# Performance work log

Measured on AMD Instinct MI355X. Metric: run time of the kernel, lower is better.

Reference implementation:

```python
import jax, jax.numpy as jnp
import numpy as np
import math

B, NMAX, PE, E, DS, NF = 8, 128, 64, 5, 64, 8  # E = num_edge_features + 1


def setup_inputs() -> dict:
    key = jax.random.key(0)
    ks = jax.random.split(key, 10)
    total = B * NMAX
    x = jax.random.normal(ks[0], (total, PE), jnp.float32)
    batch = jnp.arange(total, dtype=jnp.int32) // NMAX  # sorted graph ids, full graphs
    q = jax.random.uniform(ks[1], (B,), jnp.float32, 0.1, 0.9)  # keep sin(2*pi*q) away from 0
    s = 0.05
    return dict(
        x=x, batch=batch, q=q,
        w_attn=jax.random.normal(ks[2], (PE, 4 * E * PE), jnp.float32) * s,
        b_attn=jnp.zeros((4 * E * PE,), jnp.float32),
        w_node=jax.random.normal(ks[3], (PE, NF), jnp.float32) * s,
        b_node=jnp.zeros((NF,), jnp.float32),
        w_phi=jax.random.normal(ks[4], (DS,), jnp.float32) * s,   # Linear(1, DS) weight
        b_phi=jax.random.normal(ks[5], (DS,), jnp.float32) * s,
        w_ctx=jax.random.normal(ks[6], (DS, DS), jnp.float32) * s,  # Linear(DS, DS, bias=False)
        w_self=jax.random.normal(ks[7], (DS,), jnp.float32) * s,  # Linear(1, DS) weight
        b_self=jax.random.normal(ks[8], (DS,), jnp.float32) * s,
        w_out=jax.random.normal(ks[9], (DS,), jnp.float32) * s,   # Linear(DS, 1) weight
        b_out=jnp.zeros((), jnp.float32),
    )


def _to_dense(batch, vals, n_graphs, n_max):
    # torch_geometric.to_dense_batch for sorted batch vector
    starts = jnp.searchsorted(batch, jnp.arange(n_graphs, dtype=batch.dtype))
    pos = jnp.arange(batch.shape[0]) - starts[batch]
    dense = jnp.zeros((n_graphs, n_max, vals.shape[-1]), vals.dtype).at[batch, pos].set(vals)
    mask = jnp.zeros((n_graphs, n_max), bool).at[batch, pos].set(True)
    return dense, mask


def reference(x, batch, q, w_attn, b_attn, w_node, b_node,
              w_phi, b_phi, w_ctx, w_self, b_self, w_out, b_out):
    scale = 1.0 / math.sqrt(E * PE)
    x_hat = x @ w_node + b_node                              # (total, NF)
    proj = x @ w_attn + b_attn                               # (total, 4*E*PE)
    dense, mask = _to_dense(batch, proj, B, NMAX)            # (B, N, 4*E*PE), (B, N)
    k1, q1, k2, q2 = jnp.split(dense, 4, axis=-1)
    heads = lambda t: t.reshape(B, NMAX, E, PE).transpose(0, 2, 1, 3)  # (B, E, N, PE)
    k1, q1, k2, q2 = heads(k1), heads(q1), heads(k2), heads(q2)
    z_re = jnp.einsum('bend,bemd->benm', k1, q1) * scale     # (B, E, N, N)
    z_im = jnp.einsum('bend,bemd->benm', k2, q2) * scale
    c = jnp.cos(2.0 * math.pi * q)[:, None, None, None]
    s = jnp.sin(2.0 * math.pi * q)[:, None, None, None]
    z = z_re + z_im * (2.0 - c) / s                          # (B, E, N, N)
    eye = jnp.eye(NMAX, dtype=bool)
    edge_mask = mask[:, :, None] & mask[:, None, :] & ~eye   # (B, N, N)
    # DeepSetClassifier
    zt = z[..., None]                                        # (B, E, N, N, 1)
    phi_out = zt * w_phi + b_phi                             # (B, E, N, N, DS)
    m = edge_mask[:, None, :, :, None].astype(z.dtype)       # (B, 1, N, N, 1)
    denom = jnp.maximum(edge_mask.sum(-1).astype(z.dtype), 1.0)[:, None, :, None]  # (B,1,N,1)
    ctx = (m * phi_out).sum(3) / denom                       # (B, E, N, DS) masked neighbor mean
    h = jax.nn.gelu(zt * w_self + b_self + (ctx @ w_ctx)[:, :, :, None, :],
                    approximate=False)                        # (B, E, N, N, DS)
    e = (h * w_out).sum(-1) + b_out                          # (B, E, N, N)
    e_hat = jnp.transpose(e, (0, 3, 2, 1))                   # transpose(-1, 1) -> (B, N, N, E)
    return (e_hat, x_hat, edge_mask, mask)
```

## Files before the change

### kernel.cpp

```cpp
#include <hip/hip_runtime.h>
#include <hip/hip_bf16.h>

#define NB 8
#define NMAXN 128
#define PEH 64
#define NE 5
#define DSZ 64
#define NFEAT 8
#define TOTALN 1024
#define PCOLS 1280

#define OUT_XHAT (NB*NMAXN*NMAXN*NE)
#define OUT_EM   (OUT_XHAT + TOTALN*NFEAT)
#define OUT_MASK (OUT_EM + NB*NMAXN*NMAXN)


__global__ void k_fused1(const float* __restrict__ x, const float* __restrict__ qv,
                         const float* __restrict__ w_attn, const float* __restrict__ b_attn,
                         const float* __restrict__ w_node, const float* __restrict__ b_node,
                         const float* __restrict__ w_phi, const float* __restrict__ b_phi,
                         const float* __restrict__ w_ctx, const float* __restrict__ b_self,
                         float* __restrict__ ws, float* __restrict__ out,
                         int offZbar, int offWpc, int offC1, int offFac, int doProj)
{
    int blk = blockIdx.x, t = threadIdx.x;
    if (blk < 256) {
        if (!doProj) return;
        __shared__ float xs[4 * 64];
        int r0 = blk * 4;
        if (t < 256) xs[t] = x[r0 * PEH + t];
        __syncthreads();
        float4 b4 = *(const float4*)&b_attn[4 * t];
        float4 a0 = b4, a1 = b4, a2 = b4, a3 = b4;
        const float* wp = w_attn + 4 * t;
        #pragma unroll 4
        for (int k = 0; k < 64; k++) {
            float4 w4 = *(const float4*)&wp[k * PCOLS];
            float x0 = xs[k], x1 = xs[64 + k], x2 = xs[128 + k], x3 = xs[192 + k];
            a0.x = fmaf(x0, w4.x, a0.x); a0.y = fmaf(x0, w4.y, a0.y); a0.z = fmaf(x0, w4.z, a0.z); a0.w = fmaf(x0, w4.w, a0.w);
            a1.x = fmaf(x1, w4.x, a1.x); a1.y = fmaf(x1, w4.y, a1.y); a1.z = fmaf(x1, w4.z, a1.z); a1.w = fmaf(x1, w4.w, a1.w);
            a2.x = fmaf(x2, w4.x, a2.x); a2.y = fmaf(x2, w4.y, a2.y); a2.z = fmaf(x2, w4.z, a2.z); a2.w = fmaf(x2, w4.w, a2.w);
            a3.x = fmaf(x3, w4.x, a3.x); a3.y = fmaf(x3, w4.y, a3.y); a3.z = fmaf(x3, w4.z, a3.z); a3.w = fmaf(x3, w4.w, a3.w);
        }
        float* pr = ws + r0 * PCOLS + 4 * t;
        *(float4*)&pr[0]         = a0;
        *(float4*)&pr[PCOLS]     = a1;
        *(float4*)&pr[2 * PCOLS] = a2;
        *(float4*)&pr[3 * PCOLS] = a3;
        return;
    }
    int b2 = blk - 256;
    if (b2 < 32) {
        if (t < 256) {
            int g = b2 * 256 + t;
            int row = g >> 3, f = g & 7;
            const float* xr = x + row * PEH;
            float acc = b_node[f];
            #pragma unroll 8
            for (int k = 0; k < PEH; k++) acc = fmaf(xr[k], w_node[k * NFEAT + f], acc);
            out[OUT_XHAT + g] = acc;
        }
    } else if (b2 < 48) {
        int base = (b2 - 32) * 8192;
        for (int g = base + t; g < base + 8192; g += 320) {
            int n = (g >> 7) & 127, m = g & 127;
            out[OUT_EM + g] = (n == m) ? 0.0f : 1.0f;
        }
    } else if (b2 == 48) {
        for (int g = t; g < 1024; g += 320) out[OUT_MASK + g] = 1.0f;
    } else if (b2 == 49) {
        if (t < 64) {
            float wpv = 0.f, bpv = 0.f;
            for (int i = 0; i < 64; i++) {
                float wc = w_ctx[i * 64 + t];
                wpv = fmaf(w_phi[i], wc, wpv);
                bpv = fmaf(b_phi[i], wc, bpv);
            }
            ws[offWpc + t] = wpv;
            ws[offC1 + t]  = b_self[t] + bpv;
        } else if (t < 72) {
            int b = t - 64;
            float qq = qv[b];
            float ang = 6.2831853071795864f * qq;
            float c = cosf(ang), s = sinf(ang);
            ws[offFac + b] = (2.0f - c) / s;
        }
    } else {
        int base = (b2 - 50) * 2560;
        for (int g = t; g < 2560; g += 320) ws[offZbar + base + g] = 0.0f;
    }
}

__global__ void k_z_fast(float* __restrict__ ws, int zsF, int offZbar, int offFac)
{
    __shared__ alignas(16) float sm[8192 + 1280 + 1024];
    float* smA = sm;
    float* smQ = sm + 8192;
    float* zp  = sm + 8192 + 1280;

    int t = threadIdx.x;
    int blk = blockIdx.x;
    int ms = blk & 7, be = blk >> 3;
    int b = be / 5, e = be - 5 * b;
    float fac = ws[offFac + b];
    const float scale = 0.05590169943749474f;
    float sfac = scale * fac;

    const float* proj = ws;
    int kn = t >> 1, kkb = (t & 1) * 32;
    int qm = t & 15, qkb = (t >> 4) * 4;

    int tx = t & 7, ty = t >> 3;
    int m0 = 2 * tx, n0 = 4 * ty;
    float acc[4][2] = {};

    for (int pass = 0; pass < 2; pass++) {
        __syncthreads();
        int colK = (pass ? 640 : 0)   + e * 64;
        int colQ = (pass ? 960 : 320) + e * 64;
        float sc = pass ? sfac : scale;
        const float* prK = proj + (b * NMAXN + kn) * PCOLS + colK + kkb;
        #pragma unroll
        for (int j4 = 0; j4 < 8; j4++) {
            float4 v = *(const float4*)&prK[4 * j4];
            smA[(kkb + 4*j4 + 0) * 128 + kn] = sc * v.x;
            smA[(kkb + 4*j4 + 1) * 128 + kn] = sc * v.y;
            smA[(kkb + 4*j4 + 2) * 128 + kn] = sc * v.z;
            smA[(kkb + 4*j4 + 3) * 128 + kn] = sc * v.w;
        }
        const float* prQ = proj + (b * NMAXN + ms * 16 + qm) * PCOLS + colQ + qkb;
        {
            float4 v = *(const float4*)&prQ[0];
            smQ[(qkb + 0) * 20 + qm] = v.x;
            smQ[(qkb + 1) * 20 + qm] = v.y;
            smQ[(qkb + 2) * 20 + qm] = v.z;
            smQ[(qkb + 3) * 20 + qm] = v.w;
        }
        __syncthreads();
        for (int k = 0; k < 64; k++) {
            float4 a4 = *(const float4*)&smA[k * 128 + n0];
            float2 q2 = *(const float2*)&smQ[k * 20 + m0];
            float ar[4] = {a4.x, a4.y, a4.z, a4.w};
            #pragma unroll
            for (int r = 0; r < 4; r++) {
                acc[r][0] = fmaf(ar[r], q2.x, acc[r][0]);
                acc[r][1] = fmaf(ar[r], q2.y, acc[r][1]);
            }
        }
    }
    __syncthreads();

    __hip_bfloat16* zsb = (__hip_bfloat16*)(ws + zsF);
    float psum[4] = {0.f, 0.f, 0.f, 0.f};
    #pragma unroll
    for (int c = 0; c < 2; c++) {
        int mg = ms * 16 + m0 + c;
        union { ushort4 u; __hip_bfloat16 h[4]; } pk;
        #pragma unroll
        for (int r = 0; r < 4; r++) {
            pk.h[r] = __float2bfloat16(acc[r][c]);
            if (mg != n0 + r) psum[r] += acc[r][c];
        }
        *(ushort4*)&zsb[((b * NMAXN + mg) * NE + e) * NMAXN + n0] = pk.u;
    }
    #pragma unroll
    for (int r = 0; r < 4; r++) zp[(n0 + r) * 8 + tx] = psum[r];
    __syncthreads();
    if (t < 128) {
        float s = 0.f;
        #pragma unroll
        for (int xx = 0; xx < 8; xx++) s += zp[t * 8 + xx];
        atomicAdd(&ws[offZbar + (b * NE + e) * NMAXN + t], s);
    }
}

__device__ __forceinline__ float gelu_fast(float x) {
    float x2 = x * x;
    float w  = -1.5957691216057308f * x * fmaf(0.044715f, x2, 1.0f);
    float ew = __expf(w);
    return x * __builtin_amdgcn_rcpf(1.0f + ew);
}

__global__ void k_epi(const float* __restrict__ ws, const float* __restrict__ w_self,
                      const float* __restrict__ w_out, const float* __restrict__ b_out,
                      float* __restrict__ out,
                      int zsF, int offZbar, int offWpc, int offC1)
{
    __shared__ alignas(16) float4 cwi[64];
    int t = threadIdx.x;
    int b = blockIdx.x >> 6, mp = blockIdx.x & 63;
    int m0 = 2 * mp;
    if (t < 64)
        cwi[t] = make_float4(w_self[t], ws[offWpc + t], ws[offC1 + t], w_out[t]);
    float zbv = ws[offZbar + b * 640 + t] * (1.0f / 127.0f);
    __syncthreads();

    const __hip_bfloat16* zsb = (const __hip_bfloat16*)(ws + zsF);
    int e = t >> 7, n = t & 127;
    float zv0 = __bfloat162float(zsb[(b * NMAXN + m0) * 640 + t]);
    float zv1 = __bfloat162float(zsb[(b * NMAXN + m0 + 1) * 640 + t]);
    float bo = b_out[0];
    float a0 = bo, a1 = bo;
    #pragma unroll 8
    for (int d = 0; d < 64; d++) {
        float4 c = cwi[d];
        float zc = fmaf(zbv, c.y, c.z);
        a0 = fmaf(gelu_fast(fmaf(zv0, c.x, zc)), c.w, a0);
        a1 = fmaf(gelu_fast(fmaf(zv1, c.x, zc)), c.w, a1);
    }
    int oo = n * NE + e;
    out[(b * NMAXN + m0) * 640 + oo]     = a0;
    out[(b * NMAXN + m0 + 1) * 640 + oo] = a1;
}

__device__ __forceinline__ void z_store4(float acc[4][4], float* ws, float* zp,
                                         int zsF, int offZbar,
                                         int b, int e, int mq, int t)
{
    int tx = t & 7, ty = t >> 3;
    int m0 = 4 * tx, n0 = 4 * ty;
    __hip_bfloat16* zsb = (__hip_bfloat16*)(ws + zsF);
    float psum[4] = {0.f, 0.f, 0.f, 0.f};
    #pragma unroll
    for (int c = 0; c < 4; c++) {
        int mg = mq * 32 + m0 + c;
        union { ushort4 u; __hip_bfloat16 h[4]; } pk;
        #pragma unroll
        for (int r = 0; r < 4; r++) {
            pk.h[r] = __float2bfloat16(acc[r][c]);
            if (mg != n0 + r) psum[r] += acc[r][c];
        }
        *(ushort4*)&zsb[((b * NMAXN + mg) * NE + e) * NMAXN + n0] = pk.u;
    }
    #pragma unroll
    for (int r = 0; r < 4; r++) zp[(n0 + r) * 8 + tx] = psum[r];
    __syncthreads();
    if (t < 128) {
        float s = 0.f;
        #pragma unroll
        for (int xx = 0; xx < 8; xx++) s += zp[t * 8 + xx];
        atomicAdd(&ws[offZbar + (b * NE + e) * NMAXN + t], s);
    }
}

__global__ void k_z_slow(const float* __restrict__ x, const float* __restrict__ w_attn,
                         const float* __restrict__ b_attn, float* __restrict__ ws,
                         int zsF, int offZbar, int offFac)
{
    __shared__ alignas(16) float sm[8320 + 2304 + 1024];
    float* xsm = sm;
    float* smA = sm;
    float* smQ = sm + 8320;
    float* zp  = sm + 8320 + 2304;

    int t = threadIdx.x;
    int blk = blockIdx.x;
    int mq = blk & 3, be = blk >> 2;
    int b = be / 5, e = be - 5 * b;
    float fac = ws[offFac + b];
    const float scale = 0.05590169943749474f;
    float sfac = scale * fac;

    int kn   = t >> 1;
    int kkb  = (t & 1) * 32;
    int qm   = t & 31;
    int qkb  = (t >> 5) * 8;
    int mglo = mq * 32 + qm;

    int tx = t & 7, ty = t >> 3;
    int m0 = 4 * tx, n0 = 4 * ty;
    float acc[4][4] = {};

    for (int pass = 0; pass < 2; pass++) {
        __syncthreads();
        for (int i = t; i < 128 * 16; i += 256) {
            int n = i >> 4, dd = (i & 15) * 4;
            float4 xv = *(const float4*)&x[(b * NMAXN + n) * PEH + dd];
            float* dst = &xsm[n * 65 + dd];
            dst[0] = xv.x; dst[1] = xv.y; dst[2] = xv.z; dst[3] = xv.w;
        }
        __syncthreads();
        int colK = (pass ? 640 : 0)   + e * 64 + kkb;
        int colQ = (pass ? 960 : 320) + e * 64 + qkb;
        float rk[32], rq[8];
        #pragma unroll
        for (int j = 0; j < 32; j++) rk[j] = b_attn[colK + j];
        #pragma unroll
        for (int j = 0; j < 8; j++)  rq[j] = b_attn[colQ + j];
        for (int d = 0; d < 64; d++) {
            const float* wrow = w_attn + d * PCOLS;
            float xk = xsm[kn * 65 + d];
            float xq = xsm[mglo * 65 + d];
            #pragma unroll
            for (int j4 = 0; j4 < 8; j4++) {
                float4 w4 = *(const float4*)&wrow[colK + 4 * j4];
                rk[4*j4+0] = fmaf(xk, w4.x, rk[4*j4+0]);
                rk[4*j4+1] = fmaf(xk, w4.y, rk[4*j4+1]);
                rk[4*j4+2] = fmaf(xk, w4.z, rk[4*j4+2]);
                rk[4*j4+3] = fmaf(xk, w4.w, rk[4*j4+3]);
            }
            #pragma unroll
            for (int j4 = 0; j4 < 2; j4++) {
                float4 w4 = *(const float4*)&wrow[colQ + 4 * j4];
                rq[4*j4+0] = fmaf(xq, w4.x, rq[4*j4+0]);
                rq[4*j4+1] = fmaf(xq, w4.y, rq[4*j4+1]);
                rq[4*j4+2] = fmaf(xq, w4.z, rq[4*j4+2]);
                rq[4*j4+3] = fmaf(xq, w4.w, rq[4*j4+3]);
            }
        }
        __syncthreads();
        float sc = pass ? sfac : scale;
        #pragma unroll
        for (int j = 0; j < 32; j++) smA[(kkb + j) * 128 + kn] = sc * rk[j];
        #pragma unroll
        for (int j = 0; j < 8; j++)  smQ[(qkb + j) * 36 + qm] = rq[j];
        __syncthreads();
        for (int k = 0; k < 64; k++) {
            float4 a4 = *(const float4*)&smA[k * 128 + n0];
            float4 q4 = *(const float4*)&smQ[k * 36 + m0];
            float ar[4] = {a4.x, a4.y, a4.z, a4.w};
            float qr[4] = {q4.x, q4.y, q4.z, q4.w};
            #pragma unroll
            for (int r = 0; r < 4; r++)
                #pragma unroll
                for (int c = 0; c < 4; c++)
                    acc[r][c] = fmaf(ar[r], qr[c], acc[r][c]);
        }
    }
    __syncthreads();
    z_store4(acc, ws, zp, zsF, offZbar, b, e, mq, t);
}

__global__ void k_epi_slow(const float* __restrict__ ws, const float* __restrict__ w_self,
                           const float* __restrict__ w_out, const float* __restrict__ b_out,
                           float* __restrict__ out,
                           int zsF, int offZbar, int offWpc, int offC1)
{
    __shared__ alignas(16) float4 cwi[64];
    int t = threadIdx.x;
    int b = blockIdx.x >> 7, m = blockIdx.x & 127;
    if (t < 64)
        cwi[t] = make_float4(w_self[t], ws[offWpc + t], ws[offC1 + t], w_out[t]);
    float zbv = ws[offZbar + b * 640 + t] * (1.0f / 127.0f);
    __syncthreads();

    const __hip_bfloat16* zsb = (const __hip_bfloat16*)(ws + zsF);
    int e = t >> 7, n = t & 127;
    float zv = __bfloat162float(zsb[(b * NMAXN + m) * 640 + t]);
    float acc = b_out[0];
    #pragma unroll 8
    for (int d = 0; d < 64; d++) {
        float4 c = cwi[d];
        float arg = fmaf(zv, c.x, fmaf(zbv, c.y, c.z));
        acc = fmaf(gelu_fast(arg), c.w, acc);
    }
    out[(b * NMAXN + m) * 640 + n * NE + e] = acc;
}

extern "C" void kernel_launch(void* const* d_in, const int* in_sizes, int n_in,
                              void* d_out, int out_size, void* d_ws, size_t ws_size,
                              hipStream_t stream)
{
    const float* x      = (const float*)d_in[0];
    const float* q      = (const float*)d_in[2];
    const float* w_attn = (const float*)d_in[3];
    const float* b_attn = (const float*)d_in[4];
    const float* w_node = (const float*)d_in[5];
    const float* b_node = (const float*)d_in[6];
    const float* w_phi  = (const float*)d_in[7];
    const float* b_phi  = (const float*)d_in[8];
    const float* w_ctx  = (const float*)d_in[9];
    const float* w_self = (const float*)d_in[10];
    const float* b_self = (const float*)d_in[11];
    const float* w_out  = (const float*)d_in[12];
    const float* b_out  = (const float*)d_in[13];
    float* ws  = (float*)d_ws;
    float* out = (float*)d_out;

    const bool big = ws_size >= (size_t)(1643656 * 4 + 64);
    const int zsF     = big ? (TOTALN * PCOLS) : 0;
    const int offZbar = zsF + 327680;
    const int offWpc  = offZbar + 5120;
    const int offC1   = offWpc + 64;
    const int offFac  = offC1 + 64;

    k_fused1<<<308, 320, 0, stream>>>(x, q, w_attn, b_attn, w_node, b_node,
                                      w_phi, b_phi, w_ctx, b_self,
                                      ws, out, offZbar, offWpc, offC1, offFac, big ? 1 : 0);
    if (big) {
        k_z_fast<<<320, 256, 0, stream>>>(ws, zsF, offZbar, offFac);
        k_epi<<<512, 640, 0, stream>>>(ws, w_self, w_out, b_out, out,
                                       zsF, offZbar, offWpc, offC1);
    } else {
        k_z_slow<<<160, 256, 0, stream>>>(x, w_attn, b_attn, ws, zsF, offZbar, offFac);
        k_epi_slow<<<1024, 640, 0, stream>>>(ws, w_self, w_out, b_out, out,
                                             zsF, offZbar, offWpc, offC1);
    }
}
```

Measured before the change: 119.0 us.

## Fuse projection into z kernel and drop separate projection/setup launch

Removes the standalone projection GEMM pass and the separate z kernel. A single 193-block kernel now recomputes the K/Q projection per (batch, edge, quarter) tile from x and w_attn in registers, and also produces x_hat and the masks. Per-quarter neighbour sums are written to separate slots instead of atomically added, which removes the zero-init pass. The ctx weight precompute moves into the epilogue kernel. This cuts the launch count from three to two and avoids the round trip of the projection buffer through global memory, at the cost of redundant projection arithmetic across the m-quarters.

New measurement: 193.1 us. +62.2%, slower.

```diff
diff --git a/kernel.cpp b/kernel.cpp
--- a/kernel.cpp
+++ b/kernel.cpp
@@ -14,132 +14,104 @@
 #define OUT_EM   (OUT_XHAT + TOTALN*NFEAT)
 #define OUT_MASK (OUT_EM + NB*NMAXN*NMAXN)
 
-
-__global__ void k_fused1(const float* __restrict__ x, const float* __restrict__ qv,
-                         const float* __restrict__ w_attn, const float* __restrict__ b_attn,
-                         const float* __restrict__ w_node, const float* __restrict__ b_node,
-                         const float* __restrict__ w_phi, const float* __restrict__ b_phi,
-                         const float* __restrict__ w_ctx, const float* __restrict__ b_self,
-                         float* __restrict__ ws, float* __restrict__ out,
-                         int offZbar, int offWpc, int offC1, int offFac, int doProj)
+#define OFF_ZBAR 327680
+#define ZBAR_STRIDE 5120
+
+__global__ __launch_bounds__(512)
+void k_zfused(const float* __restrict__ x, const float* __restrict__ qv,
+              const float* __restrict__ w_attn, const float* __restrict__ b_attn,
+              const float* __restrict__ w_node, const float* __restrict__ b_node,
+              float* __restrict__ ws, float* __restrict__ out)
 {
     int blk = blockIdx.x, t = threadIdx.x;
-    if (blk < 256) {
-        if (!doProj) return;
-        __shared__ float xs[4 * 64];
-        int r0 = blk * 4;
-        if (t < 256) xs[t] = x[r0 * PEH + t];
-        __syncthreads();
-        float4 b4 = *(const float4*)&b_attn[4 * t];
-        float4 a0 = b4, a1 = b4, a2 = b4, a3 = b4;
-        const float* wp = w_attn + 4 * t;
-        #pragma unroll 4
-        for (int k = 0; k < 64; k++) {
-            float4 w4 = *(const float4*)&wp[k * PCOLS];
-            float x0 = xs[k], x1 = xs[64 + k], x2 = xs[128 + k], x3 = xs[192 + k];
-            a0.x = fmaf(x0, w4.x, a0.x); a0.y = fmaf(x0, w4.y, a0.y); a0.z = fmaf(x0, w4.z, a0.z); a0.w = fmaf(x0, w4.w, a0.w);
-            a1.x = fmaf(x1, w4.x, a1.x); a1.y = fmaf(x1, w4.y, a1.y); a1.z = fmaf(x1, w4.z, a1.z); a1.w = fmaf(x1, w4.w, a1.w);
-            a2.x = fmaf(x2, w4.x, a2.x); a2.y = fmaf(x2, w4.y, a2.y); a2.z = fmaf(x2, w4.z, a2.z); a2.w = fmaf(x2, w4.w, a2.w);
-            a3.x = fmaf(x3, w4.x, a3.x); a3.y = fmaf(x3, w4.y, a3.y); a3.z = fmaf(x3, w4.z, a3.z); a3.w = fmaf(x3, w4.w, a3.w);
-        }
-        float* pr = ws + r0 * PCOLS + 4 * t;
-        *(float4*)&pr[0]         = a0;
-        *(float4*)&pr[PCOLS]     = a1;
-        *(float4*)&pr[2 * PCOLS] = a2;
-        *(float4*)&pr[3 * PCOLS] = a3;
-        return;
-    }
-    int b2 = blk - 256;
-    if (b2 < 32) {
-        if (t < 256) {
-            int g = b2 * 256 + t;
+    if (blk >= 160) {
+        int b2 = blk - 160;
+        if (b2 < 16) {
+            int g = b2 * 512 + t;
             int row = g >> 3, f = g & 7;
             const float* xr = x + row * PEH;
             float acc = b_node[f];
             #pragma unroll 8
             for (int k = 0; k < PEH; k++) acc = fmaf(xr[k], w_node[k * NFEAT + f], acc);
             out[OUT_XHAT + g] = acc;
-        }
-    } else if (b2 < 48) {
-        int base = (b2 - 32) * 8192;
-        for (int g = base + t; g < base + 8192; g += 320) {
-            int n = (g >> 7) & 127, m = g & 127;
-            out[OUT_EM + g] = (n == m) ? 0.0f : 1.0f;
-        }
-    } else if (b2 == 48) {
-        for (int g = t; g < 1024; g += 320) out[OUT_MASK + g] = 1.0f;
-    } else if (b2 == 49) {
-        if (t < 64) {
-            float wpv = 0.f, bpv = 0.f;
-            for (int i = 0; i < 64; i++) {
-                float wc = w_ctx[i * 64 + t];
-                wpv = fmaf(w_phi[i], wc, wpv);
-                bpv = fmaf(b_phi[i], wc, bpv);
+        } else if (b2 < 32) {
+            int base = (b2 - 16) * 8192;
+            for (int g = base + t; g < base + 8192; g += 512) {
+                int n = (g >> 7) & 127, m = g & 127;
+                out[OUT_EM + g] = (n == m) ? 0.0f : 1.0f;
             }
-            ws[offWpc + t] = wpv;
-            ws[offC1 + t]  = b_self[t] + bpv;
-        } else if (t < 72) {
-            int b = t - 64;
-            float qq = qv[b];
-            float ang = 6.2831853071795864f * qq;
-            float c = cosf(ang), s = sinf(ang);
-            ws[offFac + b] = (2.0f - c) / s;
-        }
-    } else {
-        int base = (b2 - 50) * 2560;
-        for (int g = t; g < 2560; g += 320) ws[offZbar + base + g] = 0.0f;
-    }
-}
-
-__global__ void k_z_fast(float* __restrict__ ws, int zsF, int offZbar, int offFac)
-{
-    __shared__ alignas(16) float sm[8192 + 1280 + 1024];
+        } else {
+            for (int g = t; g < 1024; g += 512) out[OUT_MASK + g] = 1.0f;
+        }
+        return;
+    }
+
+    __shared__ alignas(16) float sm[8320 + 2304];
+    float* xsm = sm;
     float* smA = sm;
-    float* smQ = sm + 8192;
-    float* zp  = sm + 8192 + 1280;
-
-    int t = threadIdx.x;
-    int blk = blockIdx.x;
-    int ms = blk & 7, be = blk >> 3;
+    float* smQ = sm + 8320;
+    float* zp  = sm + 8320;
+
+    int be = blk >> 2, mq = blk & 3;
     int b = be / 5, e = be - 5 * b;
-    float fac = ws[offFac + b];
+    float ang = 6.2831853071795864f * qv[b];
+    float fac = (2.0f - cosf(ang)) / sinf(ang);
     const float scale = 0.05590169943749474f;
     float sfac = scale * fac;
 
-    const float* proj = ws;
-    int kn = t >> 1, kkb = (t & 1) * 32;
-    int qm = t & 15, qkb = (t >> 4) * 4;
-
-    int tx = t & 7, ty = t >> 3;
+    int kn = t >> 2, kkb = (t & 3) * 16;
+    int qm = t & 31, qkb = (t >> 5) * 4;
+    int qrow = mq * 32 + qm;
+
+    int tx = t & 15, ty = t >> 4;
     int m0 = 2 * tx, n0 = 4 * ty;
     float acc[4][2] = {};
 
     for (int pass = 0; pass < 2; pass++) {
         __syncthreads();
-        int colK = (pass ? 640 : 0)   + e * 64;
-        int colQ = (pass ? 960 : 320) + e * 64;
+        for (int i = t; i < 128 * 16; i += 512) {
+            int n = i >> 4, dd = (i & 15) * 4;
+            float4 xv = *(const float4*)&x[(b * NMAXN + n) * PEH + dd];
+            float* dst = &xsm[n * 65 + dd];
+            dst[0] = xv.x; dst[1] = xv.y; dst[2] = xv.z; dst[3] = xv.w;
+        }
+        __syncthreads();
+        int cK = (pass ? 640 : 0)   + e * 64 + kkb;
+        int cQ = (pass ? 960 : 320) + e * 64 + qkb;
+        float rk[16], rq[4];
+        #pragma unroll
+        for (int j = 0; j < 16; j++) rk[j] = b_attn[cK + j];
+        #pragma unroll
+        for (int j = 0; j < 4; j++)  rq[j] = b_attn[cQ + j];
+        #pragma unroll 4
+        for (int d = 0; d < 64; d++) {
+            const float* wr = w_attn + d * PCOLS;
+            float xk = xsm[kn * 65 + d];
+            float xq = xsm[qrow * 65 + d];
+            #pragma unroll
+            for (int j4 = 0; j4 < 4; j4++) {
+                float4 w4 = *(const float4*)&wr[cK + 4 * j4];
+                rk[4*j4+0] = fmaf(xk, w4.x, rk[4*j4+0]);
+                rk[4*j4+1] = fmaf(xk, w4.y, rk[4*j4+1]);
+                rk[4*j4+2] = fmaf(xk, w4.z, rk[4*j4+2]);
+                rk[4*j4+3] = fmaf(xk, w4.w, rk[4*j4+3]);
+            }
+            float4 wq = *(const float4*)&wr[cQ];
+            rq[0] = fmaf(xq, wq.x, rq[0]);
+            rq[1] = fmaf(xq, wq.y, rq[1]);
+            rq[2] = fmaf(xq, wq.z, rq[2]);
+            rq[3] = fmaf(xq, wq.w, rq[3]);
+        }
+        __syncthreads();
         float sc = pass ? sfac : scale;
-        const float* prK = proj + (b * NMAXN + kn) * PCOLS + colK + kkb;
-        #pragma unroll
-        for (int j4 = 0; j4 < 8; j4++) {
-            float4 v = *(const float4*)&prK[4 * j4];
-            smA[(kkb + 4*j4 + 0) * 128 + kn] = sc * v.x;
-            smA[(kkb + 4*j4 + 1) * 128 + kn] = sc * v.y;
-            smA[(kkb + 4*j4 + 2) * 128 + kn] = sc * v.z;
-            smA[(kkb + 4*j4 + 3) * 128 + kn] = sc * v.w;
-        }
-        const float* prQ = proj + (b * NMAXN + ms * 16 + qm) * PCOLS + colQ + qkb;
-        {
-            float4 v = *(const float4*)&prQ[0];
-            smQ[(qkb + 0) * 20 + qm] = v.x;
-            smQ[(qkb + 1) * 20 + qm] = v.y;
-            smQ[(qkb + 2) * 20 + qm] = v.z;
-            smQ[(qkb + 3) * 20 + qm] = v.w;
-        }
+        #pragma unroll
+        for (int j = 0; j < 16; j++) smA[(kkb + j) * 128 + kn] = sc * rk[j];
+        #pragma unroll
+        for (int j = 0; j < 4; j++)  smQ[(qkb + j) * 36 + qm] = rq[j];
         __syncthreads();
         for (int k = 0; k < 64; k++) {
             float4 a4 = *(const float4*)&smA[k * 128 + n0];
-            float2 q2 = *(const float2*)&smQ[k * 20 + m0];
+            float2 q2 = *(const float2*)&smQ[k * 36 + m0];
             float ar[4] = {a4.x, a4.y, a4.z, a4.w};
             #pragma unroll
             for (int r = 0; r < 4; r++) {
@@ -150,11 +122,11 @@
     }
     __syncthreads();
 
-    __hip_bfloat16* zsb = (__hip_bfloat16*)(ws + zsF);
+    __hip_bfloat16* zsb = (__hip_bfloat16*)ws;
     float psum[4] = {0.f, 0.f, 0.f, 0.f};
     #pragma unroll
     for (int c = 0; c < 2; c++) {
-        int mg = ms * 16 + m0 + c;
+        int mg = mq * 32 + m0 + c;
         union { ushort4 u; __hip_bfloat16 h[4]; } pk;
         #pragma unroll
         for (int r = 0; r < 4; r++) {
@@ -164,13 +136,13 @@
         *(ushort4*)&zsb[((b * NMAXN + mg) * NE + e) * NMAXN + n0] = pk.u;
     }
     #pragma unroll
-    for (int r = 0; r < 4; r++) zp[(n0 + r) * 8 + tx] = psum[r];
+    for (int r = 0; r < 4; r++) zp[(n0 + r) * 16 + tx] = psum[r];
     __syncthreads();
     if (t < 128) {
         float s = 0.f;
         #pragma unroll
-        for (int xx = 0; xx < 8; xx++) s += zp[t * 8 + xx];
-        atomicAdd(&ws[offZbar + (b * NE + e) * NMAXN + t], s);
+        for (int xx = 0; xx < 16; xx++) s += zp[t * 16 + xx];
+        ws[OFF_ZBAR + mq * ZBAR_STRIDE + (b * NE + e) * NMAXN + t] = s;
     }
 }
 
@@ -181,21 +153,33 @@
     return x * __builtin_amdgcn_rcpf(1.0f + ew);
 }
 
-__global__ void k_epi(const float* __restrict__ ws, const float* __restrict__ w_self,
+__global__ void k_epi(const float* __restrict__ ws,
+                      const float* __restrict__ w_phi, const float* __restrict__ b_phi,
+                      const float* __restrict__ w_ctx,
+                      const float* __restrict__ w_self, const float* __restrict__ b_self,
                       const float* __restrict__ w_out, const float* __restrict__ b_out,
-                      float* __restrict__ out,
-                      int zsF, int offZbar, int offWpc, int offC1)
+                      float* __restrict__ out)
 {
     __shared__ alignas(16) float4 cwi[64];
     int t = threadIdx.x;
     int b = blockIdx.x >> 6, mp = blockIdx.x & 63;
     int m0 = 2 * mp;
-    if (t < 64)
-        cwi[t] = make_float4(w_self[t], ws[offWpc + t], ws[offC1 + t], w_out[t]);
-    float zbv = ws[offZbar + b * 640 + t] * (1.0f / 127.0f);
+    if (t < 64) {
+        float wpv = 0.f, bpv = 0.f;
+        #pragma unroll 8
+        for (int i = 0; i < 64; i++) {
+            float wc = w_ctx[i * 64 + t];
+            wpv = fmaf(w_phi[i], wc, wpv);
+            bpv = fmaf(b_phi[i], wc, bpv);
+        }
+        cwi[t] = make_float4(w_self[t], wpv, b_self[t] + bpv, w_out[t]);
+    }
+    const float* zb = ws + OFF_ZBAR + b * 640 + t;
+    float zbv = (zb[0] + zb[ZBAR_STRIDE] + zb[2 * ZBAR_STRIDE] + zb[3 * ZBAR_STRIDE])
+                * (1.0f / 127.0f);
     __syncthreads();
 
-    const __hip_bfloat16* zsb = (const __hip_bfloat16*)(ws + zsF);
+    const __hip_bfloat16* zsb = (const __hip_bfloat16*)ws;
     int e = t >> 7, n = t & 127;
     float zv0 = __bfloat162float(zsb[(b * NMAXN + m0) * 640 + t]);
     float zv1 = __bfloat162float(zsb[(b * NMAXN + m0 + 1) * 640 + t]);
@@ -211,150 +195,6 @@
     int oo = n * NE + e;
     out[(b * NMAXN + m0) * 640 + oo]     = a0;
     out[(b * NMAXN + m0 + 1) * 640 + oo] = a1;
-}
-
-__device__ __forceinline__ void z_store4(float acc[4][4], float* ws, float* zp,
-                                         int zsF, int offZbar,
-                                         int b, int e, int mq, int t)
-{
-    int tx = t & 7, ty = t >> 3;
-    int m0 = 4 * tx, n0 = 4 * ty;
-    __hip_bfloat16* zsb = (__hip_bfloat16*)(ws + zsF);
-    float psum[4] = {0.f, 0.f, 0.f, 0.f};
-    #pragma unroll
-    for (int c = 0; c < 4; c++) {
-        int mg = mq * 32 + m0 + c;
-        union { ushort4 u; __hip_bfloat16 h[4]; } pk;
-        #pragma unroll
-        for (int r = 0; r < 4; r++) {
-            pk.h[r] = __float2bfloat16(acc[r][c]);
-            if (mg != n0 + r) psum[r] += acc[r][c];
-        }
-        *(ushort4*)&zsb[((b * NMAXN + mg) * NE + e) * NMAXN + n0] = pk.u;
-    }
-    #pragma unroll
-    for (int r = 0; r < 4; r++) zp[(n0 + r) * 8 + tx] = psum[r];
-    __syncthreads();
-    if (t < 128) {
-        float s = 0.f;
-        #pragma unroll
-        for (int xx = 0; xx < 8; xx++) s += zp[t * 8 + xx];
-        atomicAdd(&ws[offZbar + (b * NE + e) * NMAXN + t], s);
-    }
-}
-
-__global__ void k_z_slow(const float* __restrict__ x, const float* __restrict__ w_attn,
-                         const float* __restrict__ b_attn, float* __restrict__ ws,
-                         int zsF, int offZbar, int offFac)
-{
-    __shared__ alignas(16) float sm[8320 + 2304 + 1024];
-    float* xsm = sm;
-    float* smA = sm;
-    float* smQ = sm + 8320;
-    float* zp  = sm + 8320 + 2304;
-
-    int t = threadIdx.x;
-    int blk = blockIdx.x;
-    int mq = blk & 3, be = blk >> 2;
-    int b = be / 5, e = be - 5 * b;
-    float fac = ws[offFac + b];
-    const float scale = 0.05590169943749474f;
-    float sfac = scale * fac;
-
-    int kn   = t >> 1;
-    int kkb  = (t & 1) * 32;
-    int qm   = t & 31;
-    int qkb  = (t >> 5) * 8;
-    int mglo = mq * 32 + qm;
-
-    int tx = t & 7, ty = t >> 3;
-    int m0 = 4 * tx, n0 = 4 * ty;
-    float acc[4][4] = {};
-
-    for (int pass = 0; pass < 2; pass++) {
-        __syncthreads();
-        for (int i = t; i < 128 * 16; i += 256) {
-            int n = i >> 4, dd = (i & 15) * 4;
-            float4 xv = *(const float4*)&x[(b * NMAXN + n) * PEH + dd];
-            float* dst = &xsm[n * 65 + dd];
-            dst[0] = xv.x; dst[1] = xv.y; dst[2] = xv.z; dst[3] = xv.w;
-        }
-        __syncthreads();
-        int colK = (pass ? 640 : 0)   + e * 64 + kkb;
-        int colQ = (pass ? 960 : 320) + e * 64 + qkb;
-        float rk[32], rq[8];
-        #pragma unroll
-        for (int j = 0; j < 32; j++) rk[j] = b_attn[colK + j];
-        #pragma unroll
-        for (int j = 0; j < 8; j++)  rq[j] = b_attn[colQ + j];
-        for (int d = 0; d < 64; d++) {
-            const float* wrow = w_attn + d * PCOLS;
-            float xk = xsm[kn * 65 + d];
-            float xq = xsm[mglo * 65 + d];
-            #pragma unroll
-            for (int j4 = 0; j4 < 8; j4++) {
-                float4 w4 = *(const float4*)&wrow[colK + 4 * j4];
-                rk[4*j4+0] = fmaf(xk, w4.x, rk[4*j4+0]);
-                rk[4*j4+1] = fmaf(xk, w4.y, rk[4*j4+1]);
-                rk[4*j4+2] = fmaf(xk, w4.z, rk[4*j4+2]);
-                rk[4*j4+3] = fmaf(xk, w4.w, rk[4*j4+3]);
-            }
-            #pragma unroll
-            for (int j4 = 0; j4 < 2; j4++) {
-                float4 w4 = *(const float4*)&wrow[colQ + 4 * j4];
-                rq[4*j4+0] = fmaf(xq, w4.x, rq[4*j4+0]);
-                rq[4*j4+1] = fmaf(xq, w4.y, rq[4*j4+1]);
-                rq[4*j4+2] = fmaf(xq, w4.z, rq[4*j4+2]);
-                rq[4*j4+3] = fmaf(xq, w4.w, rq[4*j4+3]);
-            }
-        }
-        __syncthreads();
-        float sc = pass ? sfac : scale;
-        #pragma unroll
-        for (int j = 0; j < 32; j++) smA[(kkb + j) * 128 + kn] = sc * rk[j];
-        #pragma unroll
-        for (int j = 0; j < 8; j++)  smQ[(qkb + j) * 36 + qm] = rq[j];
-        __syncthreads();
-        for (int k = 0; k < 64; k++) {
-            float4 a4 = *(const float4*)&smA[k * 128 + n0];
-            float4 q4 = *(const float4*)&smQ[k * 36 + m0];
-            float ar[4] = {a4.x, a4.y, a4.z, a4.w};
-            float qr[4] = {q4.x, q4.y, q4.z, q4.w};
-            #pragma unroll
-            for (int r = 0; r < 4; r++)
-                #pragma unroll
-                for (int c = 0; c < 4; c++)
-                    acc[r][c] = fmaf(ar[r], qr[c], acc[r][c]);
-        }
-    }
-    __syncthreads();
-    z_store4(acc, ws, zp, zsF, offZbar, b, e, mq, t);
-}
-
-__global__ void k_epi_slow(const float* __restrict__ ws, const float* __restrict__ w_self,
-                           const float* __restrict__ w_out, const float* __restrict__ b_out,
-                           float* __restrict__ out,
-                           int zsF, int offZbar, int offWpc, int offC1)
-{
-    __shared__ alignas(16) float4 cwi[64];
-    int t = threadIdx.x;
-    int b = blockIdx.x >> 7, m = blockIdx.x & 127;
-    if (t < 64)
-        cwi[t] = make_float4(w_self[t], ws[offWpc + t], ws[offC1 + t], w_out[t]);
-    float zbv = ws[offZbar + b * 640 + t] * (1.0f / 127.0f);
-    __syncthreads();
-
-    const __hip_bfloat16* zsb = (const __hip_bfloat16*)(ws + zsF);
-    int e = t >> 7, n = t & 127;
-    float zv = __bfloat162float(zsb[(b * NMAXN + m) * 640 + t]);
-    float acc = b_out[0];
-    #pragma unroll 8
-    for (int d = 0; d < 64; d++) {
-        float4 c = cwi[d];
-        float arg = fmaf(zv, c.x, fmaf(zbv, c.y, c.z));
-        acc = fmaf(gelu_fast(arg), c.w, acc);
-    }
-    out[(b * NMAXN + m) * 640 + n * NE + e] = acc;
 }
 
 extern "C" void kernel_launch(void* const* d_in, const int* in_sizes, int n_in,
@@ -377,23 +217,6 @@
     float* ws  = (float*)d_ws;
     float* out = (float*)d_out;
 
-    const bool big = ws_size >= (size_t)(1643656 * 4 + 64);
-    const int zsF     = big ? (TOTALN * PCOLS) : 0;
-    const int offZbar = zsF + 327680;
-    const int offWpc  = offZbar + 5120;
-    const int offC1   = offWpc + 64;
-    const int offFac  = offC1 + 64;
-
-    k_fused1<<<308, 320, 0, stream>>>(x, q, w_attn, b_attn, w_node, b_node,
-                                      w_phi, b_phi, w_ctx, b_self,
-                                      ws, out, offZbar, offWpc, offC1, offFac, big ? 1 : 0);
-    if (big) {
-        k_z_fast<<<320, 256, 0, stream>>>(ws, zsF, offZbar, offFac);
-        k_epi<<<512, 640, 0, stream>>>(ws, w_self, w_out, b_out, out,
-                                       zsF, offZbar, offWpc, offC1);
-    } else {
-        k_z_slow<<<160, 256, 0, stream>>>(x, w_attn, b_attn, ws, zsF, offZbar, offFac);
-        k_epi_slow<<<1024, 640, 0, stream>>>(ws, w_self, w_out, b_out, out,
-                                             zsF, offZbar, offWpc, offC1);
-    }
-}
+    k_zfused<<<193, 512, 0, stream>>>(x, q, w_attn, b_attn, w_node, b_node, ws, out);
+    k_epi<<<512, 640, 0, stream>>>(ws, w_phi, b_phi, w_ctx, w_self, b_self, w_out, b_out, out);
+}
```
